# Kernel tuning notes

Hardware: AMD Instinct MI355X
Metric: run time of the kernel (lower is better)

Reference implementation:

```python
import jax, jax.numpy as jnp
import numpy as np
import math

B, N, DIN, H, DH, DV, DENC, MAXLEN = 8, 1024, 1024, 8, 128, 64, 32, 1024
EPS = 1e-5


def _make_pe():
    # sinusoidal table, stored as a learnable parameter in the torch module
    pos = np.arange(MAXLEN, dtype=np.float32)[:, None]
    div = np.exp(np.arange(0, DENC, 2, dtype=np.float32) * (-math.log(10000.0) / DENC))
    pe = np.zeros((MAXLEN, DENC), np.float32)
    pe[:, 0::2] = np.sin(pos * div)
    pe[:, 1::2] = np.cos(pos * div)
    return jnp.asarray(pe)[None]  # (1, MAXLEN, DENC)


def setup_inputs() -> dict:
    key = jax.random.key(0)
    ks = jax.random.split(key, 4)
    dq = DH * H  # = d_q = d_k = 1024
    return {
        "x": jax.random.normal(ks[0], (B, N, DIN), jnp.float32),
        "gamma": jnp.ones((1, 1, DIN), jnp.float32),
        "beta": jnp.zeros((1, 1, DIN), jnp.float32),
        "pe": _make_pe(),
        "W_pos": jax.random.normal(ks[1], (DIN + DENC, DIN), jnp.float32) * 0.02,
        "b_pos": jnp.zeros((DIN,), jnp.float32),
        "W_qkv": jax.random.normal(ks[2], (DIN, 2 * dq + DV * H), jnp.float32) * 0.02,
        "b_qkv": jnp.zeros((2 * dq + DV * H,), jnp.float32),
        "W_out": jax.random.normal(ks[3], (DV * H, DIN), jnp.float32) * 0.02,
        "b_out": jnp.zeros((DIN,), jnp.float32),
        "scale": jnp.asarray(1.414, jnp.float32),
    }


def reference(x, gamma, beta, pe, W_pos, b_pos, W_qkv, b_qkv, W_out, b_out, scale):
    Bq, Nq, _ = x.shape
    # PositionalEncoding: concat sinusoidal table, project back to d_in, residual add
    pos_in = jnp.concatenate([x, jnp.broadcast_to(pe[:, :Nq], (Bq, Nq, DENC))], axis=-1)
    h = x + (pos_in @ W_pos + b_pos)
    # FeatureNorm: normalize over the SEQUENCE dim (dim=1), biased variance
    mean = h.mean(axis=1, keepdims=True)
    var = h.var(axis=1, keepdims=True)
    hn = gamma * (h - mean) * jax.lax.rsqrt(var + EPS) + beta
    # QKV projection and head split
    qkv = hn @ W_qkv + b_qkv
    dq = DH * H
    q = qkv[..., :dq].reshape(Bq, Nq, H, DH).transpose(0, 2, 1, 3)       # (B,H,N,DH)
    k = qkv[..., dq:2 * dq].reshape(Bq, Nq, H, DH).transpose(0, 2, 1, 3)  # (B,H,N,DH)
    v = qkv[..., 2 * dq:].reshape(Bq, Nq, H, DV).transpose(0, 2, 1, 3)    # (B,H,N,DV)
    # for_twdit branch: attn = softmax(-(cdist(q,k)/scale)^2) == softmax(-||q-k||^2/scale^2)
    sq = jnp.sum(q * q, axis=-1)  # (B,H,N)
    sk = jnp.sum(k * k, axis=-1)  # (B,H,N)
    d2 = sq[..., :, None] + sk[..., None, :] - 2.0 * jnp.einsum('bhnc,bhmc->bhnm', q, k)
    d2 = jnp.maximum(d2, 0.0)  # cdist is a true (nonnegative) distance
    attn = jax.nn.softmax(-d2 / (scale * scale), axis=-1)  # (B,H,N,N)
    out = jnp.einsum('bhnm,bhmd->bhnd', attn, v)            # (B,H,N,DV)
    out = out.transpose(0, 2, 1, 3).reshape(Bq, Nq, H * DV)
    return x + (out @ W_out + b_out)
```

## Files before the change

### kernel.cpp

```cpp
#include <hip/hip_runtime.h>
#include <math.h>

typedef __bf16 bf16;
typedef __attribute__((ext_vector_type(8))) __bf16 bf16x8;
typedef __attribute__((ext_vector_type(4))) float f32x4;

#define MFMA16(a, b, c) __builtin_amdgcn_mfma_f32_16x16x32_bf16(a, b, c, 0, 0, 0)

__device__ __forceinline__ void gld_lds16(const void* g, void* l) {
  __builtin_amdgcn_global_load_lds(
      (const __attribute__((address_space(1))) unsigned int*)g,
      (__attribute__((address_space(3))) unsigned int*)l, 16, 0, 0);
}

__global__ __launch_bounds__(256) void prep_kernel(
    const float* __restrict__ x, const float* __restrict__ W_pos,
    const float* __restrict__ W_qkv, const float* __restrict__ W_out,
    const float* __restrict__ pe,
    bf16* __restrict__ x_bf, bf16* __restrict__ wpos_t, bf16* __restrict__ wqkv_t,
    bf16* __restrict__ wout_t, bf16* __restrict__ pe_pj) {
  __shared__ float tile[32][33];
  const int tid = threadIdx.x;
  int blk = blockIdx.x;
  if (blk < 4096) {
    int idx = blk * 256 + tid;
    const float4 a = ((const float4*)x)[idx * 2];
    const float4 b = ((const float4*)x)[idx * 2 + 1];
    bf16x8 o = {(bf16)a.x, (bf16)a.y, (bf16)a.z, (bf16)a.w,
                (bf16)b.x, (bf16)b.y, (bf16)b.z, (bf16)b.w};
    *(bf16x8*)(x_bf + (size_t)idx * 8) = o;
    return;
  }
  blk -= 4096;
  if (blk < 4096) {
    const float* W; bf16* WT; int K, N, bx, by;
    if (blk < 1024)      { W = W_pos; WT = wpos_t; K = 1024; N = 1024; bx = blk & 31; by = blk >> 5; }
    else if (blk < 3584) { int b2 = blk - 1024; W = W_qkv; WT = wqkv_t; K = 1024; N = 2560; bx = b2 % 80; by = b2 / 80; }
    else                 { int b2 = blk - 3584; W = W_out; WT = wout_t; K = 512;  N = 1024; bx = b2 & 31; by = b2 >> 5; }
    const int n0 = bx * 32, k0 = by * 32;
    const int tx = tid & 31, ty = tid >> 5;
#pragma unroll
    for (int i = 0; i < 4; ++i)
      tile[ty + 8 * i][tx] = W[(size_t)(k0 + ty + 8 * i) * N + n0 + tx];
    __syncthreads();
#pragma unroll
    for (int i = 0; i < 4; ++i)
      WT[(size_t)(n0 + ty + 8 * i) * K + k0 + tx] = (bf16)tile[tx][ty + 8 * i];
    return;
  }
  blk -= 4096;
  int idx = blk * 256 + tid;
  int n = idx >> 10, c = idx & 1023;
  float s = 0.f;
#pragma unroll
  for (int e = 0; e < 32; ++e)
    s += pe[n * 32 + e] * W_pos[(size_t)(1024 + e) * 1024 + c];
  pe_pj[idx] = (bf16)s;
}

template <int NT, int OUT_BF16>
__global__ __launch_bounds__(512) void gemm_bf16(
    const bf16* __restrict__ A, const bf16* __restrict__ BT, void* __restrict__ Cout,
    int M, int N, int K,
    const float* __restrict__ bias, const float* __restrict__ add_full,
    const bf16* __restrict__ add_mod) {
  __shared__ __align__(16) bf16 As[3][128 * 64];
  __shared__ __align__(16) bf16 Bs[3][256 * 64];
  const int tid = threadIdx.x;
  const int wave = tid >> 6, lane = tid & 63;
  const int wr = wave >> 2, wc = wave & 3;
  const int lr = lane & 15, lg = lane >> 4;

  const int nwg = gridDim.x * gridDim.y;
  const int bid = blockIdx.y * gridDim.x + blockIdx.x;
  const int s = (bid & 7) * (nwg >> 3) + (bid >> 3);
  const int row0 = (s / gridDim.x) * 128, col0 = (s % gridDim.x) * 256;

  const int trow = tid >> 3;
  const int cbd = ((tid & 7) * 16) ^ ((trow & 7) << 4);
  const bf16* asrc = A + (size_t)(row0 + trow) * K + (cbd >> 1);
  const bf16* bsrc = BT + (size_t)(col0 + trow) * K + (cbd >> 1);
  f32x4 acc[4][4] = {};

  auto STAGE = [&](int sel, int t) {
    const int kt = t * 64;
    char* al = (char*)&As[sel][0] + tid * 16;
    char* bl = (char*)&Bs[sel][0] + tid * 16;
#pragma unroll
    for (int c = 0; c < 2; ++c)
      gld_lds16(asrc + (size_t)c * 64 * K + kt, al + c * 8192);
#pragma unroll
    for (int c = 0; c < 4; ++c)
      gld_lds16(bsrc + (size_t)c * 64 * K + kt, bl + c * 8192);
  };

  STAGE(0, 0);
  STAGE(1, 1);

#pragma unroll
  for (int t = 0; t < NT; ++t) {
    if (t + 1 < NT)
      asm volatile("s_waitcnt vmcnt(6)" ::: "memory");
    else
      asm volatile("s_waitcnt vmcnt(0)" ::: "memory");
    __builtin_amdgcn_s_barrier();
    if (t + 2 < NT) STAGE((t + 2) % 3, t + 2);
    const char* Ab = (const char*)&As[t % 3][0];
    const char* Bb = (const char*)&Bs[t % 3][0];
#pragma unroll
    for (int kc = 0; kc < 2; ++kc) {
      bf16x8 af[4], bfr[4];
#pragma unroll
      for (int mt = 0; mt < 4; ++mt) {
        int r = wr * 64 + mt * 16 + lr;
        int byte = r * 128 + (((kc * 32 + lg * 8) * 2) ^ ((r & 7) << 4));
        af[mt] = *(const bf16x8*)(Ab + byte);
      }
#pragma unroll
      for (int nt = 0; nt < 4; ++nt) {
        int c = wc * 64 + nt * 16 + lr;
        int byte = c * 128 + (((kc * 32 + lg * 8) * 2) ^ ((c & 7) << 4));
        bfr[nt] = *(const bf16x8*)(Bb + byte);
      }
      __builtin_amdgcn_s_setprio(1);
#pragma unroll
      for (int mt = 0; mt < 4; ++mt)
#pragma unroll
        for (int nt = 0; nt < 4; ++nt)
          acc[mt][nt] = MFMA16(af[mt], bfr[nt], acc[mt][nt]);
      __builtin_amdgcn_s_setprio(0);
    }
  }

#pragma unroll
  for (int mt = 0; mt < 4; ++mt) {
#pragma unroll
    for (int v = 0; v < 4; ++v) {
      int r = row0 + wr * 64 + mt * 16 + lg * 4 + v;
#pragma unroll
      for (int nt = 0; nt < 4; ++nt) {
        int c = col0 + wc * 64 + nt * 16 + lr;
        float val = acc[mt][nt][v];
        if (bias) val += bias[c];
        if (add_full) val += add_full[(size_t)r * N + c];
        if (add_mod) val += (float)add_mod[(size_t)(r & 1023) * N + c];
        if (OUT_BF16)
          ((bf16*)Cout)[(size_t)r * N + c] = (bf16)val;
        else
          ((float*)Cout)[(size_t)r * N + c] = val;
      }
    }
  }
}

__global__ __launch_bounds__(512) void featnorm_kernel(const bf16* __restrict__ h,
                                                       bf16* __restrict__ hn,
                                                       const float* __restrict__ gamma,
                                                       const float* __restrict__ beta) {
  const int b = blockIdx.x >> 4;
  const int d0 = (blockIdx.x & 15) << 6;
  const int tid = threadIdx.x;
  const int c = tid & 63, g = tid >> 6;
  const size_t base = (size_t)b * (1024 * 1024) + d0 + c;
  float s = 0.f, s2 = 0.f;
  for (int n = g * 128; n < g * 128 + 128; ++n) {
    float v = (float)h[base + (size_t)n * 1024];
    s += v; s2 += v * v;
  }
  __shared__ float rs[8][64], rs2[8][64];
  rs[g][c] = s; rs2[g][c] = s2;
  __syncthreads();
  __shared__ float smean[64], srstd[64];
  if (tid < 64) {
    float S = 0.f, S2 = 0.f;
#pragma unroll
    for (int q = 0; q < 8; ++q) { S += rs[q][tid]; S2 += rs2[q][tid]; }
    float mean = S * (1.f / 1024.f);
    float var = S2 * (1.f / 1024.f) - mean * mean;
    smean[tid] = mean;
    srstd[tid] = rsqrtf(var + 1e-5f);
  }
  __syncthreads();
  const float mean = smean[c], rstd = srstd[c];
  const float gm = gamma[d0 + c], bt = beta[d0 + c];
  for (int n = g * 128; n < g * 128 + 128; ++n) {
    size_t idx = base + (size_t)n * 1024;
    hn[idx] = (bf16)(gm * ((float)h[idx] - mean) * rstd + bt);
  }
}

__global__ __launch_bounds__(256) void skvt_kernel(const bf16* __restrict__ qkv,
                                                   const float* __restrict__ scale_ptr,
                                                   float* __restrict__ skl,
                                                   bf16* __restrict__ vT) {
  const int tid = threadIdx.x;
  if (blockIdx.x < 4096) {
    const int lr = tid & 15;
    const int task = blockIdx.x * 16 + (tid >> 4);
    const int bh = task >> 10, n = task & 1023;
    const int b = bh >> 3, h = bh & 7;
    const bf16x8 v = *(const bf16x8*)(qkv + (size_t)(b * 1024 + n) * 2560 +
                                      1024 + h * 128 + lr * 8);
    float s = 0.f;
#pragma unroll
    for (int i = 0; i < 8; ++i) { float f = (float)v[i]; s += f * f; }
#pragma unroll
    for (int off = 1; off < 16; off <<= 1) s += __shfl_xor(s, off);
    if (lr == 0) {
      float sc = scale_ptr[0];
      skl[task] = s * (1.44269504f / (sc * sc));
    }
    return;
  }
  __shared__ bf16 tile[32][34];
  const int blk = blockIdx.x - 4096;
  const int b = blk >> 9;
  const int rem = blk & 511;
  const int c0 = (rem >> 5) * 32, n0 = (rem & 31) * 32;
  const int tx = tid & 31, ty = tid >> 5;
#pragma unroll
  for (int i = 0; i < 4; ++i)
    tile[ty + 8 * i][tx] = qkv[(size_t)(b * 1024 + n0 + ty + 8 * i) * 2560 + 2048 + c0 + tx];
  __syncthreads();
#pragma unroll
  for (int i = 0; i < 4; ++i)
    vT[(size_t)(b * 512 + c0 + ty + 8 * i) * 1024 + n0 + tx] = tile[tx][ty + 8 * i];
}

__global__ __launch_bounds__(512, 4) void attn_mfma(const bf16* __restrict__ qkv,
                                                    const bf16* __restrict__ vT,
                                                    const float* __restrict__ skl,
                                                    const float* __restrict__ scale_ptr,
                                                    bf16* __restrict__ attn_o) {
  const int swz = ((blockIdx.x & 7) << 6) + (blockIdx.x >> 3);
  const int it = swz & 7, bh = swz >> 3;
  const int b = bh >> 3, h = bh & 7;
  const int i0 = it * 128;
  const int tid = threadIdx.x, wave = tid >> 6, lane = tid & 63;
  const int lr = lane & 15, lg = lane >> 4;
  const float sc = scale_ptr[0];
  const float c2 = 2.f * 1.44269504f / (sc * sc);

  __shared__ __align__(16) bf16 Ks[2][64 * 128];
  __shared__ __align__(16) bf16 Vs[2][64 * 64];
  __shared__ __align__(16) bf16 Ps[8][16 * 64];
  __shared__ float sks[1024];

  const int trowK = tid >> 4;
  const int cbKd = ((tid & 15) * 16) ^ ((trowK & 7) << 4);
  const bf16* ksrc = qkv + (size_t)(b * 1024 + trowK) * 2560 + 1024 + h * 128 + (cbKd >> 1);
  const int trowV = tid >> 3;
  const int cbVd = ((tid & 7) * 16) ^ ((trowV & 7) << 4);
  const bf16* vsrc = vT + (size_t)(b * 512 + h * 64 + trowV) * 1024 + (cbVd >> 1);

  auto STAGE = [&](int sel, int jt) {
    const bf16* kp = ksrc + (size_t)jt * 64 * 2560;
    char* kl = (char*)&Ks[sel][0] + tid * 16;
    gld_lds16(kp, kl);
    gld_lds16(kp + (size_t)32 * 2560, kl + 8192);
    gld_lds16(vsrc + jt * 64, (char*)&Vs[sel][0] + tid * 16);
  };

  {
    float2 sv = ((const float2*)(skl + (size_t)bh * 1024))[tid];
    *(float2*)&sks[tid * 2] = sv;
  }
  bf16x8 qf[4];
  {
    const bf16* qrow = qkv + (size_t)(b * 1024 + i0 + wave * 16 + lr) * 2560 + h * 128;
#pragma unroll
    for (int kc = 0; kc < 4; ++kc) qf[kc] = *(const bf16x8*)(qrow + kc * 32 + lg * 8);
  }
  __syncthreads();

  bf16x8 vones;
  {
    bf16 one_or_zero = (lr == 0) ? (bf16)1.0f : (bf16)0.0f;
#pragma unroll
    for (int i = 0; i < 8; ++i) vones[i] = one_or_zero;
  }

  f32x4 o[4] = {};
  f32x4 o_l = {};

  STAGE(0, 0);
  asm volatile("s_waitcnt vmcnt(0)" ::: "memory");
  __builtin_amdgcn_s_barrier();

#pragma unroll
  for (int jt = 0; jt < 16; ++jt) {
    const int cur = jt & 1;
    if (jt < 15) STAGE(cur ^ 1, jt + 1);

    f32x4 sacc[4] = {};
    __builtin_amdgcn_s_setprio(1);
#pragma unroll
    for (int kc = 0; kc < 4; ++kc) {
#pragma unroll
      for (int nt = 0; nt < 4; ++nt) {
        int j = nt * 16 + lr;
        int byte = j * 256 + (((kc * 32 + lg * 8) * 2) ^ ((j & 7) << 4));
        bf16x8 kf = *(const bf16x8*)((const char*)&Ks[cur][0] + byte);
        sacc[nt] = MFMA16(qf[kc], kf, sacc[nt]);
      }
    }
    __builtin_amdgcn_s_setprio(0);

#pragma unroll
    for (int nt = 0; nt < 4; ++nt) {
      float skv = sks[jt * 64 + nt * 16 + lr];
#pragma unroll
      for (int v = 0; v < 4; ++v) {
        float p = __builtin_amdgcn_exp2f(sacc[nt][v] * c2 - skv);
        int r = lg * 4 + v, c = nt * 16 + lr;
        int byte = r * 128 + ((c * 2) ^ ((r & 7) << 4));
        *(bf16*)((char*)&Ps[wave][0] + byte) = (bf16)p;
      }
    }
    bf16x8 pf[2];
#pragma unroll
    for (int kc = 0; kc < 2; ++kc) {
      int byte = lr * 128 + (((kc * 32 + lg * 8) * 2) ^ ((lr & 7) << 4));
      pf[kc] = *(const bf16x8*)((const char*)&Ps[wave][0] + byte);
    }
    __builtin_amdgcn_s_setprio(1);
#pragma unroll
    for (int kc = 0; kc < 2; ++kc) {
#pragma unroll
      for (int nt = 0; nt < 4; ++nt) {
        int d = nt * 16 + lr;
        int byte = d * 128 + (((kc * 32 + lg * 8) * 2) ^ ((d & 7) << 4));
        bf16x8 vf = *(const bf16x8*)((const char*)&Vs[cur][0] + byte);
        o[nt] = MFMA16(pf[kc], vf, o[nt]);
      }
      o_l = MFMA16(pf[kc], vones, o_l);
    }
    __builtin_amdgcn_s_setprio(0);

    asm volatile("s_waitcnt vmcnt(0)" ::: "memory");
    __builtin_amdgcn_s_barrier();
  }

#pragma unroll
  for (int v = 0; v < 4; ++v) {
    float ls = __shfl(o_l[v], lg << 4);
    float inv = 1.f / ls;
    int r = i0 + wave * 16 + lg * 4 + v;
#pragma unroll
    for (int nt = 0; nt < 4; ++nt) {
      int c = h * 64 + nt * 16 + lr;
      attn_o[(size_t)(b * 1024 + r) * 512 + c] = (bf16)(o[nt][v] * inv);
    }
  }
}

extern "C" void kernel_launch(void* const* d_in, const int* in_sizes, int n_in,
                              void* d_out, int out_size, void* d_ws, size_t ws_size,
                              hipStream_t stream) {
  const float* x     = (const float*)d_in[0];
  const float* gamma = (const float*)d_in[1];
  const float* beta  = (const float*)d_in[2];
  const float* pe    = (const float*)d_in[3];
  const float* W_pos = (const float*)d_in[4];
  const float* b_pos = (const float*)d_in[5];
  const float* W_qkv = (const float*)d_in[6];
  const float* b_qkv = (const float*)d_in[7];
  const float* W_out = (const float*)d_in[8];
  const float* b_out = (const float*)d_in[9];
  const float* scale = (const float*)d_in[10];
  float* outp = (float*)d_out;

  char* ws = (char*)d_ws;
  const size_t MB = 1 << 20;
  bf16* x_bf   = (bf16*)(ws);
  bf16* hn     = (bf16*)(ws);
  bf16* wpos_t = (bf16*)(ws + 16 * MB);
  bf16* wqkv_t = (bf16*)(ws + 18 * MB);
  bf16* wout_t = (bf16*)(ws + 23 * MB);
  bf16* pe_pj  = (bf16*)(ws + 24 * MB);
  bf16* vT     = (bf16*)(ws + 24 * MB);
  bf16* h      = (bf16*)(ws + 32 * MB);
  bf16* attn_o = (bf16*)(ws + 32 * MB);
  bf16* qkv    = (bf16*)(ws + 48 * MB);
  float* skl   = (float*)(ws + 88 * MB);

  prep_kernel<<<12288, 256, 0, stream>>>(x, W_pos, W_qkv, W_out, pe,
                                         x_bf, wpos_t, wqkv_t, wout_t, pe_pj);
  gemm_bf16<16, 1><<<dim3(4, 64), 512, 0, stream>>>(x_bf, wpos_t, h, 8192, 1024, 1024,
                                                    b_pos, x, pe_pj);
  featnorm_kernel<<<128, 512, 0, stream>>>(h, hn, gamma, beta);
  gemm_bf16<16, 1><<<dim3(10, 64), 512, 0, stream>>>(hn, wqkv_t, qkv, 8192, 2560, 1024,
                                                     b_qkv, nullptr, nullptr);
  skvt_kernel<<<8192, 256, 0, stream>>>(qkv, scale, skl, vT);
  attn_mfma<<<512, 512, 0, stream>>>(qkv, vT, skl, scale, attn_o);
  gemm_bf16<8, 0><<<dim3(4, 64), 512, 0, stream>>>(attn_o, wout_t, outp, 8192, 1024, 512,
                                                   b_out, x, nullptr);
}
```

Before: 257.1 us.

## Restructure GEMM into 8-phase ping-pong pipeline with quadrant MFMA scheduling

Replaces the triple-buffered GEMM with a double-buffered kernel that splits each k-tile into four quadrant MFMA phases. LDS fragment reads and half-tile global-to-LDS loads are interleaved between the phases, with barriers separating them. The QKV projection now uses a 256-row tile with a halved grid, and launch bounds pin one block per SM. The goal is better overlap of memory and MFMA work and more reuse per block, at the cost of many extra barriers and a larger register footprint.

```diff
diff --git a/kernel.cpp b/kernel.cpp
--- a/kernel.cpp
+++ b/kernel.cpp
@@ -11,6 +11,13 @@
   __builtin_amdgcn_global_load_lds(
       (const __attribute__((address_space(1))) unsigned int*)g,
       (__attribute__((address_space(3))) unsigned int*)l, 16, 0, 0);
+}
+
+template <int N>
+__device__ __forceinline__ void vmwait() {
+  if constexpr (N == 0) asm volatile("s_waitcnt vmcnt(0)" ::: "memory");
+  else if constexpr (N == 3) asm volatile("s_waitcnt vmcnt(3)" ::: "memory");
+  else if constexpr (N == 4) asm volatile("s_waitcnt vmcnt(4)" ::: "memory");
 }
 
 __global__ __launch_bounds__(256) void prep_kernel(
@@ -58,14 +65,23 @@
   pe_pj[idx] = (bf16)s;
 }
 
-template <int NT, int OUT_BF16>
-__global__ __launch_bounds__(512) void gemm_bf16(
+template <int BM, int NT, int OUT_BF16>
+__global__ __launch_bounds__(512, 1) void gemm8p(
     const bf16* __restrict__ A, const bf16* __restrict__ BT, void* __restrict__ Cout,
     int M, int N, int K,
     const float* __restrict__ bias, const float* __restrict__ add_full,
     const bf16* __restrict__ add_mod) {
-  __shared__ __align__(16) bf16 As[3][128 * 64];
-  __shared__ __align__(16) bf16 Bs[3][256 * 64];
+  constexpr int MT = BM / 32;
+  constexpr int MH = MT / 2;
+  constexpr int LA = BM / 128;
+  constexpr int LB = 2;
+  constexpr int ABYTES = BM * 128;
+  constexpr int BBYTES = 256 * 128;
+  constexpr int VM1 = LA + LB;
+
+  __shared__ __align__(16) bf16 As[2][BM * 64];
+  __shared__ __align__(16) bf16 Bs[2][256 * 64];
+
   const int tid = threadIdx.x;
   const int wave = tid >> 6, lane = tid & 63;
   const int wr = wave >> 2, wc = wave & 3;
@@ -73,70 +89,131 @@
 
   const int nwg = gridDim.x * gridDim.y;
   const int bid = blockIdx.y * gridDim.x + blockIdx.x;
-  const int s = (bid & 7) * (nwg >> 3) + (bid >> 3);
-  const int row0 = (s / gridDim.x) * 128, col0 = (s % gridDim.x) * 256;
-
-  const int trow = tid >> 3;
-  const int cbd = ((tid & 7) * 16) ^ ((trow & 7) << 4);
-  const bf16* asrc = A + (size_t)(row0 + trow) * K + (cbd >> 1);
-  const bf16* bsrc = BT + (size_t)(col0 + trow) * K + (cbd >> 1);
-  f32x4 acc[4][4] = {};
-
-  auto STAGE = [&](int sel, int t) {
-    const int kt = t * 64;
-    char* al = (char*)&As[sel][0] + tid * 16;
-    char* bl = (char*)&Bs[sel][0] + tid * 16;
-#pragma unroll
-    for (int c = 0; c < 2; ++c)
-      gld_lds16(asrc + (size_t)c * 64 * K + kt, al + c * 8192);
-#pragma unroll
-    for (int c = 0; c < 4; ++c)
-      gld_lds16(bsrc + (size_t)c * 64 * K + kt, bl + c * 8192);
+  const int sw = (bid & 7) * (nwg >> 3) + (bid >> 3);
+  const int row0 = (sw / gridDim.x) * BM, col0 = (sw % gridDim.x) * 256;
+
+  const int cbS = ((tid & 7) * 16) ^ (((tid >> 3) & 7) << 4);
+  const bf16* asrc = A + (size_t)(row0 + (tid >> 3)) * K + (cbS >> 1);
+  const bf16* bsrc = BT + (size_t)(col0 + (tid >> 3)) * K + (cbS >> 1);
+
+  f32x4 acc[MT][4] = {};
+
+  auto stageA = [&](int sel, int t, int half) {
+#pragma unroll
+    for (int i = 0; i < LA; ++i)
+      gld_lds16(asrc + (size_t)(half * (BM / 2) + i * 64) * K + t * 64,
+                (char*)As + sel * ABYTES + half * (BM / 2 * 128) + i * 8192 + tid * 16);
   };
-
-  STAGE(0, 0);
-  STAGE(1, 1);
+  auto stageB = [&](int sel, int t, int half) {
+#pragma unroll
+    for (int i = 0; i < LB; ++i)
+      gld_lds16(bsrc + (size_t)(half * 128 + i * 64) * K + t * 64,
+                (char*)Bs + sel * BBYTES + half * 16384 + i * 8192 + tid * 16);
+  };
+
+  stageB(0, 0, 0); stageA(0, 0, 0); stageB(0, 0, 1); stageA(0, 0, 1);
+  stageB(1, 1, 0); stageA(1, 1, 0);
+  vmwait<VM1>();
+  __builtin_amdgcn_s_barrier();
 
 #pragma unroll
   for (int t = 0; t < NT; ++t) {
-    if (t + 1 < NT)
-      asm volatile("s_waitcnt vmcnt(6)" ::: "memory");
-    else
-      asm volatile("s_waitcnt vmcnt(0)" ::: "memory");
-    __builtin_amdgcn_s_barrier();
-    if (t + 2 < NT) STAGE((t + 2) % 3, t + 2);
-    const char* Ab = (const char*)&As[t % 3][0];
-    const char* Bb = (const char*)&Bs[t % 3][0];
-#pragma unroll
-    for (int kc = 0; kc < 2; ++kc) {
-      bf16x8 af[4], bfr[4];
-#pragma unroll
-      for (int mt = 0; mt < 4; ++mt) {
-        int r = wr * 64 + mt * 16 + lr;
-        int byte = r * 128 + (((kc * 32 + lg * 8) * 2) ^ ((r & 7) << 4));
-        af[mt] = *(const bf16x8*)(Ab + byte);
-      }
-#pragma unroll
-      for (int nt = 0; nt < 4; ++nt) {
-        int c = wc * 64 + nt * 16 + lr;
-        int byte = c * 128 + (((kc * 32 + lg * 8) * 2) ^ ((c & 7) << 4));
-        bfr[nt] = *(const bf16x8*)(Bb + byte);
-      }
-      __builtin_amdgcn_s_setprio(1);
-#pragma unroll
-      for (int mt = 0; mt < 4; ++mt)
-#pragma unroll
-        for (int nt = 0; nt < 4; ++nt)
-          acc[mt][nt] = MFMA16(af[mt], bfr[nt], acc[mt][nt]);
-      __builtin_amdgcn_s_setprio(0);
-    }
-  }
-
-#pragma unroll
-  for (int mt = 0; mt < 4; ++mt) {
+    const int buf = t & 1;
+    const char* Ab = (const char*)As + buf * ABYTES;
+    const char* Bb = (const char*)Bs + buf * BBYTES;
+    bf16x8 aLo[MH][2], aHi[MH][2], bLo[2][2], bHi[2][2];
+
+#pragma unroll
+    for (int m = 0; m < MH; ++m)
+#pragma unroll
+      for (int kc = 0; kc < 2; ++kc) {
+        int r = wr * (BM / 2) + m * 16 + lr;
+        aLo[m][kc] = *(const bf16x8*)(Ab + r * 128 + ((kc * 64 + lg * 16) ^ ((r & 7) << 4)));
+      }
+#pragma unroll
+    for (int n = 0; n < 2; ++n)
+#pragma unroll
+      for (int kc = 0; kc < 2; ++kc) {
+        int r = wc * 64 + n * 16 + lr;
+        bLo[n][kc] = *(const bf16x8*)(Bb + r * 128 + ((kc * 64 + lg * 16) ^ ((r & 7) << 4)));
+      }
+    if (t + 1 < NT) stageB(buf ^ 1, t + 1, 1);
+    __builtin_amdgcn_s_barrier();
+    asm volatile("s_waitcnt lgkmcnt(0)" ::: "memory");
+    __builtin_amdgcn_s_setprio(1);
+#pragma unroll
+    for (int m = 0; m < MH; ++m)
+#pragma unroll
+      for (int n = 0; n < 2; ++n)
+#pragma unroll
+        for (int kc = 0; kc < 2; ++kc)
+          acc[m][n] = MFMA16(aLo[m][kc], bLo[n][kc], acc[m][n]);
+    __builtin_amdgcn_s_setprio(0);
+    __builtin_amdgcn_s_barrier();
+
+#pragma unroll
+    for (int n = 0; n < 2; ++n)
+#pragma unroll
+      for (int kc = 0; kc < 2; ++kc) {
+        int r = wc * 64 + (2 + n) * 16 + lr;
+        bHi[n][kc] = *(const bf16x8*)(Bb + r * 128 + ((kc * 64 + lg * 16) ^ ((r & 7) << 4)));
+      }
+    if (t + 1 < NT) stageA(buf ^ 1, t + 1, 1);
+    __builtin_amdgcn_s_barrier();
+    asm volatile("s_waitcnt lgkmcnt(0)" ::: "memory");
+    __builtin_amdgcn_s_setprio(1);
+#pragma unroll
+    for (int m = 0; m < MH; ++m)
+#pragma unroll
+      for (int n = 0; n < 2; ++n)
+#pragma unroll
+        for (int kc = 0; kc < 2; ++kc)
+          acc[m][2 + n] = MFMA16(aLo[m][kc], bHi[n][kc], acc[m][2 + n]);
+    __builtin_amdgcn_s_setprio(0);
+    __builtin_amdgcn_s_barrier();
+
+#pragma unroll
+    for (int m = 0; m < MH; ++m)
+#pragma unroll
+      for (int kc = 0; kc < 2; ++kc) {
+        int r = wr * (BM / 2) + (MH + m) * 16 + lr;
+        aHi[m][kc] = *(const bf16x8*)(Ab + r * 128 + ((kc * 64 + lg * 16) ^ ((r & 7) << 4)));
+      }
+    if (t + 2 < NT) stageB(buf, t + 2, 0);
+    __builtin_amdgcn_s_barrier();
+    asm volatile("s_waitcnt lgkmcnt(0)" ::: "memory");
+    __builtin_amdgcn_s_setprio(1);
+#pragma unroll
+    for (int m = 0; m < MH; ++m)
+#pragma unroll
+      for (int n = 0; n < 2; ++n)
+#pragma unroll
+        for (int kc = 0; kc < 2; ++kc)
+          acc[MH + m][2 + n] = MFMA16(aHi[m][kc], bHi[n][kc], acc[MH + m][2 + n]);
+    __builtin_amdgcn_s_setprio(0);
+    __builtin_amdgcn_s_barrier();
+
+    if (t + 2 < NT) stageA(buf, t + 2, 0);
+    __builtin_amdgcn_s_barrier();
+    __builtin_amdgcn_s_setprio(1);
+#pragma unroll
+    for (int m = 0; m < MH; ++m)
+#pragma unroll
+      for (int n = 0; n < 2; ++n)
+#pragma unroll
+        for (int kc = 0; kc < 2; ++kc)
+          acc[MH + m][n] = MFMA16(aHi[m][kc], bLo[n][kc], acc[MH + m][n]);
+    __builtin_amdgcn_s_setprio(0);
+    if (t + 2 < NT) vmwait<VM1>();
+    else if (t + 1 < NT) vmwait<0>();
+    __builtin_amdgcn_s_barrier();
+  }
+
+#pragma unroll
+  for (int mt = 0; mt < MT; ++mt) {
 #pragma unroll
     for (int v = 0; v < 4; ++v) {
-      int r = row0 + wr * 64 + mt * 16 + lg * 4 + v;
+      int r = row0 + wr * (BM / 2) + mt * 16 + lg * 4 + v;
 #pragma unroll
       for (int nt = 0; nt < 4; ++nt) {
         int c = col0 + wc * 64 + nt * 16 + lr;
@@ -386,13 +463,13 @@
 
   prep_kernel<<<12288, 256, 0, stream>>>(x, W_pos, W_qkv, W_out, pe,
                                          x_bf, wpos_t, wqkv_t, wout_t, pe_pj);
-  gemm_bf16<16, 1><<<dim3(4, 64), 512, 0, stream>>>(x_bf, wpos_t, h, 8192, 1024, 1024,
-                                                    b_pos, x, pe_pj);
+  gemm8p<128, 16, 1><<<dim3(4, 64), 512, 0, stream>>>(x_bf, wpos_t, h, 8192, 1024, 1024,
+                                                      b_pos, x, pe_pj);
   featnorm_kernel<<<128, 512, 0, stream>>>(h, hn, gamma, beta);
-  gemm_bf16<16, 1><<<dim3(10, 64), 512, 0, stream>>>(hn, wqkv_t, qkv, 8192, 2560, 1024,
-                                                     b_qkv, nullptr, nullptr);
+  gemm8p<256, 16, 1><<<dim3(10, 32), 512, 0, stream>>>(hn, wqkv_t, qkv, 8192, 2560, 1024,
+                                                       b_qkv, nullptr, nullptr);
   skvt_kernel<<<8192, 256, 0, stream>>>(qkv, scale, skl, vT);
   attn_mfma<<<512, 512, 0, stream>>>(qkv, vT, skl, scale, attn_o);
-  gemm_bf16<8, 0><<<dim3(4, 64), 512, 0, stream>>>(attn_o, wout_t, outp, 8192, 1024, 512,
-                                                   b_out, x, nullptr);
-}
+  gemm8p<128, 8, 0><<<dim3(4, 64), 512, 0, stream>>>(attn_o, wout_t, outp, 8192, 1024, 512,
+                                                     b_out, x, nullptr);
+}
```

Result: slower. 316.9 us (+23.3%).
